# Kernel optimization log

Hardware: AMD Instinct MI355X
Metric: run time of the kernel (lower is better)

Reference implementation:

```python
import jax, jax.numpy as jnp
import numpy as np

TURBO_BLOCK_SIZE = 64
TURBO_MSE_BITS = 5
QMAX = 2 ** (TURBO_MSE_BITS - 1) - 1  # 15 for symmetric int5
# MSE scale search grid: shrink factors applied to the max-abs scale
SHRINKS = np.linspace(0.4, 1.0, 16)


def mse_quant_dequant(w):
    """Block-wise (block=64, along input dim) symmetric int5 quantize-dequantize.
    Per block, searches a grid of shrunken max-abs scales and keeps the one
    minimizing reconstruction MSE."""
    O, I = w.shape
    wb = w.reshape(O, I // TURBO_BLOCK_SIZE, TURBO_BLOCK_SIZE)
    amax = jnp.max(jnp.abs(wb), axis=-1, keepdims=True)
    base = jnp.maximum(amax, 1e-8) / QMAX
    best_err = jnp.full(amax.shape, jnp.inf, dtype=w.dtype)
    best_scale = base
    for s in SHRINKS:  # fixed small grid, not a data-dim loop
        scale = base * jnp.asarray(s, dtype=w.dtype)
        deq = jnp.clip(jnp.round(wb / scale), -QMAX, QMAX) * scale
        err = jnp.sum((deq - wb) ** 2, axis=-1, keepdims=True)
        upd = err < best_err
        best_err = jnp.where(upd, err, best_err)
        best_scale = jnp.where(upd, scale, best_scale)
    deq = jnp.clip(jnp.round(wb / best_scale), -QMAX, QMAX) * best_scale
    return deq.reshape(O, I)


def turbo_linear(x, w):
    # Straight-through estimator: forward uses quantized weights,
    # gradient flows to w as identity.
    wq = w + jax.lax.stop_gradient(mse_quant_dequant(w) - w)
    return x @ wq.T


def setup_inputs() -> dict:
    key = jax.random.key(0)
    k1, k2, k3 = jax.random.split(key, 3)
    dim, mlp_mult = 2048, 4
    hidden = mlp_mult * dim
    x = jax.random.normal(k1, (4, 2048, dim), dtype=jnp.float32)
    w_fc = jax.random.normal(k2, (hidden, dim), dtype=jnp.float32) * 0.02
    w_proj = jax.random.normal(k3, (dim, hidden), dtype=jnp.float32) * 0.02
    return {"x": x, "w_fc": w_fc, "w_proj": w_proj}


def reference(x, w_fc, w_proj):
    h = jnp.maximum(turbo_linear(x, w_fc), 0.0)  # relu
    return turbo_linear(h * h, w_proj)           # relu-square then proj
```

## Files before the change

### kernel.cpp

```cpp
#include <hip/hip_runtime.h>
#include <hip/hip_bf16.h>

typedef __attribute__((ext_vector_type(8))) __bf16 bf16x8;
typedef __attribute__((ext_vector_type(4))) float f32x4;

__device__ __forceinline__ void gload_lds16(const void* g, void* lds) {
    __builtin_amdgcn_global_load_lds(
        (const __attribute__((address_space(1))) void*)g,
        (__attribute__((address_space(3))) void*)lds, 16, 0, 0);
}

__global__ __launch_bounds__(256) void quant_bf16_kernel(
    const float* __restrict__ w, __hip_bfloat16* __restrict__ wq, int nblk)
{
#pragma clang fp contract(off)
    int b = blockIdx.x * 256 + threadIdx.x;
    if (b >= nblk) return;
    const float4* src = (const float4*)(w + (size_t)b * 64);
    float v[64];
#pragma unroll
    for (int i = 0; i < 16; ++i) {
        float4 t = src[i];
        v[i*4+0] = t.x; v[i*4+1] = t.y; v[i*4+2] = t.z; v[i*4+3] = t.w;
    }
    float amax = 0.0f;
#pragma unroll
    for (int i = 0; i < 64; ++i) amax = fmaxf(amax, fabsf(v[i]));
    float base = fmaxf(amax, 1e-8f) / 15.0f;

    float best_err = __builtin_inff();
    float best_scale = base, best_rs = 0.0f;
    for (int k = 0; k < 16; ++k) {
        double sd = (k == 15) ? 1.0 : ((double)k * (0.6 / 15.0) + 0.4);
        float scale = base * (float)sd;
        float rs = 1.0f / scale;
        float err = 0.0f;
#pragma unroll
        for (int i = 0; i < 64; ++i) {
            float q = rintf(v[i] * rs);
            q = fminf(fmaxf(q, -15.0f), 15.0f);
            float d = q * scale - v[i];
            err = err + d * d;
        }
        if (err < best_err) { best_err = err; best_scale = scale; best_rs = rs; }
    }
    __hip_bfloat16* dst = wq + (size_t)b * 64;
#pragma unroll
    for (int i = 0; i < 64; ++i) {
        float q = rintf(v[i] * best_rs);
        q = fminf(fmaxf(q, -15.0f), 15.0f);
        dst[i] = __float2bfloat16(q * best_scale);
    }
}

__global__ __launch_bounds__(256) void f32_to_bf16_kernel(
    const float* __restrict__ in, __hip_bfloat16* __restrict__ out, int n8)
{
    int i = blockIdx.x * 256 + threadIdx.x;
    if (i >= n8) return;
    const float4* p = (const float4*)(in + (size_t)i * 8);
    float4 a = p[0], b = p[1];
    alignas(16) __hip_bfloat16 r[8];
    r[0] = __float2bfloat16(a.x); r[1] = __float2bfloat16(a.y);
    r[2] = __float2bfloat16(a.z); r[3] = __float2bfloat16(a.w);
    r[4] = __float2bfloat16(b.x); r[5] = __float2bfloat16(b.y);
    r[6] = __float2bfloat16(b.z); r[7] = __float2bfloat16(b.w);
    *(uint4*)(out + (size_t)i * 8) = *(const uint4*)r;
}

#define LDA2(d, base, s) { \
    d[0] = *(const bf16x8*)(smem + (base) + aB + (s)*2048u + cb0); \
    d[1] = *(const bf16x8*)(smem + (base) + aB + (s)*2048u + cb1); }

#define LDB8(base) { \
    bf[0][0] = *(const bf16x8*)(smem + (base) + bB + 0u    + cb0); \
    bf[0][1] = *(const bf16x8*)(smem + (base) + bB + 0u    + cb1); \
    bf[1][0] = *(const bf16x8*)(smem + (base) + bB + 2048u + cb0); \
    bf[1][1] = *(const bf16x8*)(smem + (base) + bB + 2048u + cb1); \
    bf[2][0] = *(const bf16x8*)(smem + (base) + bB + 4096u + cb0); \
    bf[2][1] = *(const bf16x8*)(smem + (base) + bB + 4096u + cb1); \
    bf[3][0] = *(const bf16x8*)(smem + (base) + bB + 6144u + cb0); \
    bf[3][1] = *(const bf16x8*)(smem + (base) + bB + 6144u + cb1); }

#define MF8(q, a2) { \
    acc[q][0] = __builtin_amdgcn_mfma_f32_16x16x32_bf16(a2[0], bf[0][0], acc[q][0],0,0,0); \
    acc[q][0] = __builtin_amdgcn_mfma_f32_16x16x32_bf16(a2[1], bf[0][1], acc[q][0],0,0,0); \
    acc[q][1] = __builtin_amdgcn_mfma_f32_16x16x32_bf16(a2[0], bf[1][0], acc[q][1],0,0,0); \
    acc[q][1] = __builtin_amdgcn_mfma_f32_16x16x32_bf16(a2[1], bf[1][1], acc[q][1],0,0,0); \
    acc[q][2] = __builtin_amdgcn_mfma_f32_16x16x32_bf16(a2[0], bf[2][0], acc[q][2],0,0,0); \
    acc[q][2] = __builtin_amdgcn_mfma_f32_16x16x32_bf16(a2[1], bf[2][1], acc[q][2],0,0,0); \
    acc[q][3] = __builtin_amdgcn_mfma_f32_16x16x32_bf16(a2[0], bf[3][0], acc[q][3],0,0,0); \
    acc[q][3] = __builtin_amdgcn_mfma_f32_16x16x32_bf16(a2[1], bf[3][1], acc[q][3],0,0,0); }

#define STAGE(base, eoff, ldsOff) \
    gload_lds16((base) + (size_t)((eoff) + voff), smem + (ldsOff) + wOff)

#define BARRIER() { __builtin_amdgcn_sched_barrier(0); \
    __builtin_amdgcn_s_barrier(); __builtin_amdgcn_sched_barrier(0); }

template <int EPI>
__global__ __launch_bounds__(512, 1) void gemm256_kernel(
    const __hip_bfloat16* __restrict__ A,
    const __hip_bfloat16* __restrict__ B,
    void* __restrict__ Cout, int M, int N, int K)
{
    extern __shared__ char smem[];

    const int t    = threadIdx.x;
    const int lane = t & 63;
    const int w    = t >> 6;
    const int wr   = w >> 2;
    const int wc   = w & 3;
    const int lo   = lane & 15;
    const int hi   = lane >> 4;
    const uint wOff = (uint)w * 1024u;

    const int cpx = gridDim.x >> 3;
    int bid = blockIdx.x;
    bid = (bid & 7) * cpx + (bid >> 3);
    const int nN = N >> 8;
    const int bm = bid / nN;
    const int bn = bid % nN;
    const int rowBase = bm << 8;
    const int colBase = bn << 8;

    const __hip_bfloat16* uA = A + (size_t)rowBase * (size_t)K;
    const __hip_bfloat16* uB = B + (size_t)colBase * (size_t)K;
    uint o0 = (uint)t * 16u;
    uint p0 = o0 ^ (((o0 >> 7) & 7u) << 4);
    const uint voff = (p0 >> 7) * (uint)K + ((p0 & 127u) >> 1);
    const uint K64 = (uint)K * 64u;

    const uint sw  = (uint)(lo & 7) << 4;
    const uint aB  = (uint)wr * 16384u + (uint)lo * 128u;
    const uint bB  = 32768u + (uint)(wc >> 1) * 16384u
                   + ((uint)(wc & 1) * 64u + (uint)lo) * 128u;
    const uint cb0 = ((uint)hi * 16u) ^ sw;
    const uint cb1 = (64u + (uint)hi * 16u) ^ sw;

    f32x4 acc[8][4] = {};
    bf16x8 aC0[2], aC1[2], bf[4][2];

    STAGE(uA, 0u,     0u);      STAGE(uA, K64,    8192u);
    STAGE(uA, 2u*K64, 16384u);  STAGE(uA, 3u*K64, 24576u);
    STAGE(uB, 0u,     32768u);  STAGE(uB, K64,    40960u);
    STAGE(uB, 2u*K64, 49152u);  STAGE(uB, 3u*K64, 57344u);
    asm volatile("s_waitcnt vmcnt(0)" ::: "memory");
    BARRIER();

    const int NT = K >> 6;
    for (int tt = 0; tt < NT; ++tt) {
        const uint bufOff = (uint)(tt & 1) * 65536u;
        const uint nxtOff = bufOff ^ 65536u;
        const bool pf = (tt + 1 < NT);
        const uint kN = ((uint)(tt + 1)) << 6;

        if (pf) {
            STAGE(uA, kN,          nxtOff + 0u);
            STAGE(uA, kN + K64,    nxtOff + 8192u);
            STAGE(uA, kN + 2u*K64, nxtOff + 16384u);
            STAGE(uA, kN + 3u*K64, nxtOff + 24576u);
            STAGE(uB, kN,          nxtOff + 32768u);
            STAGE(uB, kN + K64,    nxtOff + 40960u);
            STAGE(uB, kN + 2u*K64, nxtOff + 49152u);
            STAGE(uB, kN + 3u*K64, nxtOff + 57344u);
        }
        __builtin_amdgcn_sched_barrier(0);

        LDB8(bufOff);
        LDA2(aC0, bufOff, 0u); LDA2(aC1, bufOff, 1u);

        __builtin_amdgcn_s_setprio(1);
        MF8(0, aC0); LDA2(aC0, bufOff, 2u);
        MF8(1, aC1); LDA2(aC1, bufOff, 3u);
        __builtin_amdgcn_s_setprio(0);

        __builtin_amdgcn_s_setprio(1);
        MF8(2, aC0); LDA2(aC0, bufOff, 4u);
        MF8(3, aC1); LDA2(aC1, bufOff, 5u);
        __builtin_amdgcn_s_setprio(0);

        __builtin_amdgcn_s_setprio(1);
        MF8(4, aC0); LDA2(aC0, bufOff, 6u);
        MF8(5, aC1); LDA2(aC1, bufOff, 7u);
        __builtin_amdgcn_s_setprio(0);

        __builtin_amdgcn_s_setprio(1);
        MF8(6, aC0);
        MF8(7, aC1);
        __builtin_amdgcn_s_setprio(0);

        if (pf) asm volatile("s_waitcnt vmcnt(0)" ::: "memory");
        BARRIER();
    }

    if (EPI == 0) {
        __hip_bfloat16* Cb = (__hip_bfloat16*)Cout;
#pragma unroll
        for (int i = 0; i < 8; ++i)
#pragma unroll
            for (int j = 0; j < 4; ++j)
#pragma unroll
                for (int r = 0; r < 4; ++r) {
                    size_t row = rowBase + wr*128 + i*16 + hi*4 + r;
                    size_t col = colBase + wc*64 + j*16 + lo;
                    float v = fmaxf(acc[i][j][r], 0.0f);
                    Cb[row * N + col] = __float2bfloat16(v * v);
                }
    } else {
        float* Cf = (float*)Cout;
#pragma unroll
        for (int i = 0; i < 8; ++i)
#pragma unroll
            for (int j = 0; j < 4; ++j)
#pragma unroll
                for (int r = 0; r < 4; ++r) {
                    size_t row = rowBase + wr*128 + i*16 + hi*4 + r;
                    size_t col = colBase + wc*64 + j*16 + lo;
                    Cf[row * N + col] = acc[i][j][r];
                }
    }
}

extern "C" void kernel_launch(void* const* d_in, const int* in_sizes, int n_in,
                              void* d_out, int out_size, void* d_ws, size_t ws_size,
                              hipStream_t stream) {
    const float* x      = (const float*)d_in[0];
    const float* w_fc   = (const float*)d_in[1];
    const float* w_proj = (const float*)d_in[2];
    float* out = (float*)d_out;

    const int DIM = 2048, HID = 8192, M = 8192;

    char* ws = (char*)d_ws;
    __hip_bfloat16* Xb  = (__hip_bfloat16*)ws;
    __hip_bfloat16* Wfc = (__hip_bfloat16*)(ws + (size_t)M * DIM * 2);
    __hip_bfloat16* Wpj = (__hip_bfloat16*)(ws + (size_t)(M * DIM + (size_t)HID * DIM) * 2);
    __hip_bfloat16* H2  = (__hip_bfloat16*)(ws + (size_t)(M * DIM + 2 * (size_t)HID * DIM) * 2);

    (void)hipFuncSetAttribute((const void*)gemm256_kernel<0>,
                              hipFuncAttributeMaxDynamicSharedMemorySize, 131072);
    (void)hipFuncSetAttribute((const void*)gemm256_kernel<1>,
                              hipFuncAttributeMaxDynamicSharedMemorySize, 131072);

    int nblk = HID * DIM / 64;
    quant_bf16_kernel<<<nblk / 256, 256, 0, stream>>>(w_fc, Wfc, nblk);
    quant_bf16_kernel<<<nblk / 256, 256, 0, stream>>>(w_proj, Wpj, nblk);

    int n8 = M * DIM / 8;
    f32_to_bf16_kernel<<<n8 / 256, 256, 0, stream>>>(x, Xb, n8);

    gemm256_kernel<0><<<(M/256)*(HID/256), 512, 131072, stream>>>(
        Xb, Wfc, (void*)H2, M, HID, DIM);

    gemm256_kernel<1><<<(M/256)*(DIM/256), 512, 131072, stream>>>(
        H2, Wpj, (void*)out, M, DIM, HID);
}
```

Baseline: 606.6 us.

## Switch GEMM to 32x32x16 MFMA with new LDS layout and interleaved reads

```diff
diff --git a/kernel.cpp b/kernel.cpp
--- a/kernel.cpp
+++ b/kernel.cpp
@@ -2,7 +2,7 @@
 #include <hip/hip_bf16.h>
 
 typedef __attribute__((ext_vector_type(8))) __bf16 bf16x8;
-typedef __attribute__((ext_vector_type(4))) float f32x4;
+typedef __attribute__((ext_vector_type(16))) float f32x16;
 
 __device__ __forceinline__ void gload_lds16(const void* g, void* lds) {
     __builtin_amdgcn_global_load_lds(
@@ -68,33 +68,40 @@
     *(uint4*)(out + (size_t)i * 8) = *(const uint4*)r;
 }
 
-#define LDA2(d, base, s) { \
-    d[0] = *(const bf16x8*)(smem + (base) + aB + (s)*2048u + cb0); \
-    d[1] = *(const bf16x8*)(smem + (base) + aB + (s)*2048u + cb1); }
-
-#define LDB8(base) { \
-    bf[0][0] = *(const bf16x8*)(smem + (base) + bB + 0u    + cb0); \
-    bf[0][1] = *(const bf16x8*)(smem + (base) + bB + 0u    + cb1); \
-    bf[1][0] = *(const bf16x8*)(smem + (base) + bB + 2048u + cb0); \
-    bf[1][1] = *(const bf16x8*)(smem + (base) + bB + 2048u + cb1); \
-    bf[2][0] = *(const bf16x8*)(smem + (base) + bB + 4096u + cb0); \
-    bf[2][1] = *(const bf16x8*)(smem + (base) + bB + 4096u + cb1); \
-    bf[3][0] = *(const bf16x8*)(smem + (base) + bB + 6144u + cb0); \
-    bf[3][1] = *(const bf16x8*)(smem + (base) + bB + 6144u + cb1); }
-
-#define MF8(q, a2) { \
-    acc[q][0] = __builtin_amdgcn_mfma_f32_16x16x32_bf16(a2[0], bf[0][0], acc[q][0],0,0,0); \
-    acc[q][0] = __builtin_amdgcn_mfma_f32_16x16x32_bf16(a2[1], bf[0][1], acc[q][0],0,0,0); \
-    acc[q][1] = __builtin_amdgcn_mfma_f32_16x16x32_bf16(a2[0], bf[1][0], acc[q][1],0,0,0); \
-    acc[q][1] = __builtin_amdgcn_mfma_f32_16x16x32_bf16(a2[1], bf[1][1], acc[q][1],0,0,0); \
-    acc[q][2] = __builtin_amdgcn_mfma_f32_16x16x32_bf16(a2[0], bf[2][0], acc[q][2],0,0,0); \
-    acc[q][2] = __builtin_amdgcn_mfma_f32_16x16x32_bf16(a2[1], bf[2][1], acc[q][2],0,0,0); \
-    acc[q][3] = __builtin_amdgcn_mfma_f32_16x16x32_bf16(a2[0], bf[3][0], acc[q][3],0,0,0); \
-    acc[q][3] = __builtin_amdgcn_mfma_f32_16x16x32_bf16(a2[1], bf[3][1], acc[q][3],0,0,0); }
-
-#define STAGE(base, eoff, ldsOff) \
-    gload_lds16((base) + (size_t)((eoff) + voff), smem + (ldsOff) + wOff)
-
+#define RDA(dst, bufOff, s) { \
+    dst[0] = *(const bf16x8*)(smem + (bufOff) + aBase + 0u*4096u + (s)*1024u); \
+    dst[1] = *(const bf16x8*)(smem + (bufOff) + aBase + 1u*4096u + (s)*1024u); \
+    dst[2] = *(const bf16x8*)(smem + (bufOff) + aBase + 2u*4096u + (s)*1024u); \
+    dst[3] = *(const bf16x8*)(smem + (bufOff) + aBase + 3u*4096u + (s)*1024u); }
+
+#define RDB(dst, bufOff, s) { \
+    dst[0] = *(const bf16x8*)(smem + (bufOff) + bBase + 0u*4096u + (s)*1024u); \
+    dst[1] = *(const bf16x8*)(smem + (bufOff) + bBase + 1u*4096u + (s)*1024u); }
+
+#define MFMA8(aS, bS) { \
+    acc[0][0] = __builtin_amdgcn_mfma_f32_32x32x16_bf16(aS[0], bS[0], acc[0][0],0,0,0); \
+    acc[0][1] = __builtin_amdgcn_mfma_f32_32x32x16_bf16(aS[0], bS[1], acc[0][1],0,0,0); \
+    acc[1][0] = __builtin_amdgcn_mfma_f32_32x32x16_bf16(aS[1], bS[0], acc[1][0],0,0,0); \
+    acc[1][1] = __builtin_amdgcn_mfma_f32_32x32x16_bf16(aS[1], bS[1], acc[1][1],0,0,0); \
+    acc[2][0] = __builtin_amdgcn_mfma_f32_32x32x16_bf16(aS[2], bS[0], acc[2][0],0,0,0); \
+    acc[2][1] = __builtin_amdgcn_mfma_f32_32x32x16_bf16(aS[2], bS[1], acc[2][1],0,0,0); \
+    acc[3][0] = __builtin_amdgcn_mfma_f32_32x32x16_bf16(aS[3], bS[0], acc[3][0],0,0,0); \
+    acc[3][1] = __builtin_amdgcn_mfma_f32_32x32x16_bf16(aS[3], bS[1], acc[3][1],0,0,0); }
+
+#define STAGE_ALL(dstOff, kElem) { \
+    gload_lds16(uA + (size_t)(voff + (kElem) + 0u*K64i), smem + (dstOff) + 0u*8192u + wOff); \
+    gload_lds16(uA + (size_t)(voff + (kElem) + 1u*K64i), smem + (dstOff) + 1u*8192u + wOff); \
+    gload_lds16(uA + (size_t)(voff + (kElem) + 2u*K64i), smem + (dstOff) + 2u*8192u + wOff); \
+    gload_lds16(uA + (size_t)(voff + (kElem) + 3u*K64i), smem + (dstOff) + 3u*8192u + wOff); \
+    gload_lds16(uB + (size_t)(voff + (kElem) + 0u*K64i), smem + (dstOff) + 32768u + 0u*8192u + wOff); \
+    gload_lds16(uB + (size_t)(voff + (kElem) + 1u*K64i), smem + (dstOff) + 32768u + 1u*8192u + wOff); \
+    gload_lds16(uB + (size_t)(voff + (kElem) + 2u*K64i), smem + (dstOff) + 32768u + 2u*8192u + wOff); \
+    gload_lds16(uB + (size_t)(voff + (kElem) + 3u*K64i), smem + (dstOff) + 32768u + 3u*8192u + wOff); }
+
+#define LGKM6() { asm volatile("s_waitcnt lgkmcnt(6)" ::: "memory"); \
+    __builtin_amdgcn_sched_barrier(0); }
+#define LGKM0() { asm volatile("s_waitcnt lgkmcnt(0)" ::: "memory"); \
+    __builtin_amdgcn_sched_barrier(0); }
 #define BARRIER() { __builtin_amdgcn_sched_barrier(0); \
     __builtin_amdgcn_s_barrier(); __builtin_amdgcn_sched_barrier(0); }
 
@@ -111,8 +118,8 @@
     const int w    = t >> 6;
     const int wr   = w >> 2;
     const int wc   = w & 3;
-    const int lo   = lane & 15;
-    const int hi   = lane >> 4;
+    const int l5   = lane & 31;
+    const int h2   = lane >> 5;
     const uint wOff = (uint)w * 1024u;
 
     const int cpx = gridDim.x >> 3;
@@ -126,25 +133,19 @@
 
     const __hip_bfloat16* uA = A + (size_t)rowBase * (size_t)K;
     const __hip_bfloat16* uB = B + (size_t)colBase * (size_t)K;
-    uint o0 = (uint)t * 16u;
-    uint p0 = o0 ^ (((o0 >> 7) & 7u) << 4);
-    const uint voff = (p0 >> 7) * (uint)K + ((p0 & 127u) >> 1);
-    const uint K64 = (uint)K * 64u;
-
-    const uint sw  = (uint)(lo & 7) << 4;
-    const uint aB  = (uint)wr * 16384u + (uint)lo * 128u;
-    const uint bB  = 32768u + (uint)(wc >> 1) * 16384u
-                   + ((uint)(wc & 1) * 64u + (uint)lo) * 128u;
-    const uint cb0 = ((uint)hi * 16u) ^ sw;
-    const uint cb1 = (64u + (uint)hi * 16u) ^ sw;
-
-    f32x4 acc[8][4] = {};
-    bf16x8 aC0[2], aC1[2], bf[4][2];
-
-    STAGE(uA, 0u,     0u);      STAGE(uA, K64,    8192u);
-    STAGE(uA, 2u*K64, 16384u);  STAGE(uA, 3u*K64, 24576u);
-    STAGE(uB, 0u,     32768u);  STAGE(uB, K64,    40960u);
-    STAGE(uB, 2u*K64, 49152u);  STAGE(uB, 3u*K64, 57344u);
+
+    const uint rS   = ((uint)(t >> 8)) * 32u + (uint)(t & 31);
+    const uint octS = ((uint)(t >> 5)) & 7u;
+    const uint voff = rS * (uint)K + octS * 8u;
+    const uint K64i = (uint)K * 64u;
+
+    const uint aBase = (uint)(wr * 4) * 4096u + (uint)h2 * 512u + (uint)l5 * 16u;
+    const uint bBase = 32768u + (uint)(wc * 2) * 4096u + (uint)h2 * 512u + (uint)l5 * 16u;
+
+    f32x16 acc[4][2] = {};
+    bf16x8 a0[4], a1[4], b0[2], b1[2];
+
+    STAGE_ALL(0u, 0u);
     asm volatile("s_waitcnt vmcnt(0)" ::: "memory");
     BARRIER();
 
@@ -155,40 +156,23 @@
         const bool pf = (tt + 1 < NT);
         const uint kN = ((uint)(tt + 1)) << 6;
 
-        if (pf) {
-            STAGE(uA, kN,          nxtOff + 0u);
-            STAGE(uA, kN + K64,    nxtOff + 8192u);
-            STAGE(uA, kN + 2u*K64, nxtOff + 16384u);
-            STAGE(uA, kN + 3u*K64, nxtOff + 24576u);
-            STAGE(uB, kN,          nxtOff + 32768u);
-            STAGE(uB, kN + K64,    nxtOff + 40960u);
-            STAGE(uB, kN + 2u*K64, nxtOff + 49152u);
-            STAGE(uB, kN + 3u*K64, nxtOff + 57344u);
-        }
-        __builtin_amdgcn_sched_barrier(0);
-
-        LDB8(bufOff);
-        LDA2(aC0, bufOff, 0u); LDA2(aC1, bufOff, 1u);
-
-        __builtin_amdgcn_s_setprio(1);
-        MF8(0, aC0); LDA2(aC0, bufOff, 2u);
-        MF8(1, aC1); LDA2(aC1, bufOff, 3u);
-        __builtin_amdgcn_s_setprio(0);
-
-        __builtin_amdgcn_s_setprio(1);
-        MF8(2, aC0); LDA2(aC0, bufOff, 4u);
-        MF8(3, aC1); LDA2(aC1, bufOff, 5u);
-        __builtin_amdgcn_s_setprio(0);
-
-        __builtin_amdgcn_s_setprio(1);
-        MF8(4, aC0); LDA2(aC0, bufOff, 6u);
-        MF8(5, aC1); LDA2(aC1, bufOff, 7u);
-        __builtin_amdgcn_s_setprio(0);
-
-        __builtin_amdgcn_s_setprio(1);
-        MF8(6, aC0);
-        MF8(7, aC1);
-        __builtin_amdgcn_s_setprio(0);
+        RDA(a0, bufOff, 0u); RDB(b0, bufOff, 0u);
+        if (pf) STAGE_ALL(nxtOff, kN);
+        RDA(a1, bufOff, 1u); RDB(b1, bufOff, 1u);
+
+        LGKM6();
+        __builtin_amdgcn_s_setprio(1); MFMA8(a0, b0); __builtin_amdgcn_s_setprio(0);
+        RDA(a0, bufOff, 2u); RDB(b0, bufOff, 2u);
+
+        LGKM6();
+        __builtin_amdgcn_s_setprio(1); MFMA8(a1, b1); __builtin_amdgcn_s_setprio(0);
+        RDA(a1, bufOff, 3u); RDB(b1, bufOff, 3u);
+
+        LGKM6();
+        __builtin_amdgcn_s_setprio(1); MFMA8(a0, b0); __builtin_amdgcn_s_setprio(0);
+
+        LGKM0();
+        __builtin_amdgcn_s_setprio(1); MFMA8(a1, b1); __builtin_amdgcn_s_setprio(0);
 
         if (pf) asm volatile("s_waitcnt vmcnt(0)" ::: "memory");
         BARRIER();
@@ -197,27 +181,27 @@
     if (EPI == 0) {
         __hip_bfloat16* Cb = (__hip_bfloat16*)Cout;
 #pragma unroll
-        for (int i = 0; i < 8; ++i)
-#pragma unroll
-            for (int j = 0; j < 4; ++j)
-#pragma unroll
-                for (int r = 0; r < 4; ++r) {
-                    size_t row = rowBase + wr*128 + i*16 + hi*4 + r;
-                    size_t col = colBase + wc*64 + j*16 + lo;
-                    float v = fmaxf(acc[i][j][r], 0.0f);
+        for (int m = 0; m < 4; ++m)
+#pragma unroll
+            for (int n = 0; n < 2; ++n)
+#pragma unroll
+                for (int r = 0; r < 16; ++r) {
+                    size_t row = rowBase + wr*128 + m*32 + (r & 3) + 8*(r >> 2) + 4*h2;
+                    size_t col = colBase + wc*64 + n*32 + l5;
+                    float v = fmaxf(acc[m][n][r], 0.0f);
                     Cb[row * N + col] = __float2bfloat16(v * v);
                 }
     } else {
         float* Cf = (float*)Cout;
 #pragma unroll
-        for (int i = 0; i < 8; ++i)
-#pragma unroll
-            for (int j = 0; j < 4; ++j)
-#pragma unroll
-                for (int r = 0; r < 4; ++r) {
-                    size_t row = rowBase + wr*128 + i*16 + hi*4 + r;
-                    size_t col = colBase + wc*64 + j*16 + lo;
-                    Cf[row * N + col] = acc[i][j][r];
+        for (int m = 0; m < 4; ++m)
+#pragma unroll
+            for (int n = 0; n < 2; ++n)
+#pragma unroll
+                for (int r = 0; r < 16; ++r) {
+                    size_t row = rowBase + wr*128 + m*32 + (r & 3) + 8*(r >> 2) + 4*h2;
+                    size_t col = colBase + wc*64 + n*32 + l5;
+                    Cf[row * N + col] = acc[m][n][r];
                 }
     }
 }
```

New measurement: 769.2 us. +26.8%, slower.
